# Kernel optimization log

Hardware: AMD Instinct MI355X
Metric: run time of the kernel (lower is better)

The kernel has to match this reference:

```python
import jax, jax.numpy as jnp
import numpy as np

N_NODES = 50000
N_EDGES = 800000
D = 64            # NODE_FEATURE_DIM == EDGE_FEATURE_DIM
H = 128           # EDGE_FEATURE_HIDDEN
EDGE_STEPS = 4
NODE_STEPS = 2


def _mlp2(h, W1, b1, W2, b2):
    # two-layer MLP with ReLU between (bn=False, end_with_relu=False)
    return jnp.maximum(h @ W1 + b1, 0.0) @ W2 + b2


def setup_inputs() -> dict:
    key = jax.random.key(0)
    ks = iter(jax.random.split(key, 40))

    def w(shape):
        fan_in = shape[0]
        return jax.random.normal(next(ks), shape, dtype=jnp.float32) / np.sqrt(fan_in)

    inp = {
        "x": jax.random.normal(next(ks), (N_NODES, 128), dtype=jnp.float32),
        "edge_attr": jax.random.normal(next(ks), (N_EDGES, 19), dtype=jnp.float32),
        "edge_index": jax.random.randint(next(ks), (2, N_EDGES), 0, N_NODES),
        "node_types": jax.random.randint(next(ks), (N_NODES,), 0, 17),
        # node embedding MLP: 128 -> 64 -> 64
        "ne_W1": w((128, D)), "ne_b1": jnp.zeros((D,)), "ne_W2": w((D, D)), "ne_b2": jnp.zeros((D,)),
        # edge embedding MLP: 19 -> 64 -> 64
        "ee_W1": w((19, D)), "ee_b1": jnp.zeros((D,)), "ee_W2": w((D, D)), "ee_b2": jnp.zeros((D,)),
        # MPN edge MLP: [x_src(2D), x_dst(2D), e(2D)] = 384 -> 128 -> 64
        "mp_eW1": w((6 * D, H)), "mp_eb1": jnp.zeros((H,)), "mp_eW2": w((H, D)), "mp_eb2": jnp.zeros((D,)),
        # MPN node-update MLP: 64 -> 64
        "mp_nW": w((D, D)), "mp_nb": jnp.zeros((D,)),
        # edge classification head: 64 -> 32 -> 1
        "ec_W1": w((D, 32)), "ec_b1": jnp.zeros((32,)), "ec_W2": w((32, 1)), "ec_b2": jnp.zeros((1,)),
        # node classification head: 64 -> 32 -> 1
        "nc_W1": w((D, 32)), "nc_b1": jnp.zeros((32,)), "nc_W2": w((32, 1)), "nc_b2": jnp.zeros((1,)),
        # type classification head: 64 -> 32 -> 17
        "cl_W1": w((D, 32)), "cl_b1": jnp.zeros((32,)), "cl_W2": w((32, 17)), "cl_b2": jnp.zeros((17,)),
    }
    return inp


def reference(x, edge_attr, edge_index, node_types,
              ne_W1, ne_b1, ne_W2, ne_b2,
              ee_W1, ee_b1, ee_W2, ee_b2,
              mp_eW1, mp_eb1, mp_eW2, mp_eb2,
              mp_nW, mp_nb,
              ec_W1, ec_b1, ec_W2, ec_b2,
              nc_W1, nc_b1, nc_W2, nc_b2,
              cl_W1, cl_b1, cl_W2, cl_b2):
    src, dst = edge_index[0], edge_index[1]

    nf0 = _mlp2(x, ne_W1, ne_b1, ne_W2, ne_b2)          # [N, D] initial node emb
    ef0 = _mlp2(edge_attr, ee_W1, ee_b1, ee_W2, ee_b2)  # [E, D] initial edge emb
    nf, ef = nf0, ef0

    def mpn_step(nf, ef):
        # skip connections: concat initial features each iteration
        nf_c = jnp.concatenate([nf0, nf], axis=1)   # [N, 2D]
        ef_c = jnp.concatenate([ef0, ef], axis=1)   # [E, 2D]
        msg_in = jnp.concatenate([nf_c[src], nf_c[dst], ef_c], axis=1)  # [E, 6D]
        e_new = _mlp2(msg_in, mp_eW1, mp_eb1, mp_eW2, mp_eb2)           # [E, D]
        agg = jax.ops.segment_sum(e_new, dst, num_segments=N_NODES)    # [N, D]
        n_new = jnp.maximum(agg @ mp_nW + mp_nb, 0.0)                   # [N, D]
        return n_new, e_new

    for _ in range(EDGE_STEPS):
        nf, ef = mpn_step(nf, ef)
    pred_edge = _mlp2(ef, ec_W1, ec_b1, ec_W2, ec_b2).squeeze(-1)  # [E]

    for _ in range(NODE_STEPS):
        nf, ef = mpn_step(nf, ef)
    pred_node = _mlp2(nf, nc_W1, nc_b1, nc_W2, nc_b2).squeeze(-1)  # [N]
    pred_class = _mlp2(nf, cl_W1, cl_b1, cl_W2, cl_b2)             # [N, 17]

    return (pred_edge, pred_node, pred_class)
```

## Files before the change

kernel.cpp:

```cpp
#include <hip/hip_runtime.h>

#define NN 50000
#define EE 800000

typedef unsigned short u16;
typedef __attribute__((ext_vector_type(8))) short bf16x8;
typedef __attribute__((ext_vector_type(4))) float f32x4;

#define MFMA16(a, b, c) __builtin_amdgcn_mfma_f32_16x16x32_bf16(a, b, c, 0, 0, 0)

__device__ __forceinline__ float bf2f(u16 v) {
    union { unsigned u; float f; } x; x.u = ((unsigned)v) << 16; return x.f;
}
__device__ __forceinline__ u16 f2bf(float f) {
    union { float f; unsigned u; } x; x.f = f;
    unsigned r = x.u + 0x7FFFu + ((x.u >> 16) & 1u);
    return (u16)(r >> 16);
}
__device__ __forceinline__ void gl_lds16(const u16* g, u16* l) {
    __builtin_amdgcn_global_load_lds((const __attribute__((address_space(1))) void*)g,
                                     (__attribute__((address_space(3))) void*)l, 16, 0, 0);
}

__global__ void pack_frag(const float* __restrict__ W, u16* __restrict__ dst, int K, int N) {
    int i = blockIdx.x * 256 + threadIdx.x;
    int nfc = N / 16, kkc = (K + 31) / 32;
    int total = kkc * nfc * 512;
    if (i >= total) return;
    int t = i & 7, lane = (i >> 3) & 63;
    int rest = i >> 9;
    int nf = rest % nfc, kk = rest / nfc;
    int k = kk * 32 + (lane >> 4) * 8 + t, n = nf * 16 + (lane & 15);
    dst[i] = (k < K) ? f2bf(W[k * N + n]) : (u16)0;
}

__global__ __launch_bounds__(256) void embed_mfma_node(
    const float* __restrict__ x, const u16* __restrict__ pW1, const float* __restrict__ b1,
    const u16* __restrict__ pW2, const float* __restrict__ b2, u16* __restrict__ out)
{
    __shared__ alignas(16) u16 A[64 * 136];
    __shared__ alignas(16) u16 Hs[64 * 72];
    int tid = threadIdx.x;
    size_t row0 = (size_t)blockIdx.x * 64;
    #pragma unroll
    for (int it = 0; it < 8; ++it) {
        int u = it * 256 + tid;
        int row = u >> 5, seg = u & 31;
        float4 v = (row0 + row < NN) ? *(const float4*)(x + (row0 + row) * 128 + seg * 4)
                                     : make_float4(0.f, 0.f, 0.f, 0.f);
        ushort4 o; o.x = f2bf(v.x); o.y = f2bf(v.y); o.z = f2bf(v.z); o.w = f2bf(v.w);
        *(ushort4*)(A + row * 136 + seg * 4) = o;
    }
    __syncthreads();
    int wave = tid >> 6, lane = tid & 63, l15 = lane & 15, l4 = lane >> 4;
    int col = wave * 16 + l15;
    f32x4 acc[4] = {};
    #pragma unroll
    for (int kk = 0; kk < 4; ++kk) {
        bf16x8 b = *(const bf16x8*)(pW1 + (size_t)((kk * 4 + wave) * 64 + lane) * 8);
        #pragma unroll
        for (int mi = 0; mi < 4; ++mi) {
            bf16x8 a = *(const bf16x8*)(A + (mi * 16 + l15) * 136 + kk * 32 + l4 * 8);
            acc[mi] = MFMA16(a, b, acc[mi]);
        }
    }
    float bias = b1[col];
    #pragma unroll
    for (int mi = 0; mi < 4; ++mi)
        #pragma unroll
        for (int r = 0; r < 4; ++r) {
            float v = acc[mi][r] + bias;
            Hs[(mi * 16 + l4 * 4 + r) * 72 + col] = f2bf(v > 0.f ? v : 0.f);
        }
    __syncthreads();
    f32x4 acc2[4] = {};
    #pragma unroll
    for (int kk = 0; kk < 2; ++kk) {
        bf16x8 b = *(const bf16x8*)(pW2 + (size_t)((kk * 4 + wave) * 64 + lane) * 8);
        #pragma unroll
        for (int mi = 0; mi < 4; ++mi) {
            bf16x8 a = *(const bf16x8*)(Hs + (mi * 16 + l15) * 72 + kk * 32 + l4 * 8);
            acc2[mi] = MFMA16(a, b, acc2[mi]);
        }
    }
    float bias2 = b2[col];
    __syncthreads();
    #pragma unroll
    for (int mi = 0; mi < 4; ++mi)
        #pragma unroll
        for (int r = 0; r < 4; ++r)
            Hs[(mi * 16 + l4 * 4 + r) * 72 + col] = f2bf(acc2[mi][r] + bias2);
    __syncthreads();
    #pragma unroll
    for (int it = 0; it < 4; ++it) {
        int u = it * 256 + tid;
        int row = u >> 4, c4 = (u & 15) * 4;
        if (row0 + row < NN) {
            ushort4 o = *(const ushort4*)(Hs + row * 72 + c4);
            *(ushort4*)(out + (row0 + row) * 64 + c4) = o;
        }
    }
}

__global__ __launch_bounds__(256) void embed_mfma_edge(
    const float* __restrict__ ea, const int* __restrict__ eids,
    const u16* __restrict__ pW1, const float* __restrict__ b1,
    const u16* __restrict__ pW2, const float* __restrict__ b2, u16* __restrict__ out)
{
    __shared__ alignas(16) u16 A[64 * 40];
    __shared__ alignas(16) u16 Hs[64 * 72];
    __shared__ int eid_s[64];
    int tid = threadIdx.x;
    size_t row0 = (size_t)blockIdx.x * 64;
    if (tid < 64) eid_s[tid] = eids[row0 + tid];
    __syncthreads();
    #pragma unroll
    for (int it = 0; it < 8; ++it) {
        int u = it * 256 + tid;
        int row = u >> 5, k = u & 31;
        float v = (k < 19) ? ea[(size_t)eid_s[row] * 19 + k] : 0.f;
        A[row * 40 + k] = f2bf(v);
    }
    __syncthreads();
    int wave = tid >> 6, lane = tid & 63, l15 = lane & 15, l4 = lane >> 4;
    int col = wave * 16 + l15;
    f32x4 acc[4] = {};
    {
        bf16x8 b = *(const bf16x8*)(pW1 + (size_t)(wave * 64 + lane) * 8);
        #pragma unroll
        for (int mi = 0; mi < 4; ++mi) {
            bf16x8 a = *(const bf16x8*)(A + (mi * 16 + l15) * 40 + l4 * 8);
            acc[mi] = MFMA16(a, b, acc[mi]);
        }
    }
    float bias = b1[col];
    #pragma unroll
    for (int mi = 0; mi < 4; ++mi)
        #pragma unroll
        for (int r = 0; r < 4; ++r) {
            float v = acc[mi][r] + bias;
            Hs[(mi * 16 + l4 * 4 + r) * 72 + col] = f2bf(v > 0.f ? v : 0.f);
        }
    __syncthreads();
    f32x4 acc2[4] = {};
    #pragma unroll
    for (int kk = 0; kk < 2; ++kk) {
        bf16x8 b = *(const bf16x8*)(pW2 + (size_t)((kk * 4 + wave) * 64 + lane) * 8);
        #pragma unroll
        for (int mi = 0; mi < 4; ++mi) {
            bf16x8 a = *(const bf16x8*)(Hs + (mi * 16 + l15) * 72 + kk * 32 + l4 * 8);
            acc2[mi] = MFMA16(a, b, acc2[mi]);
        }
    }
    float bias2 = b2[col];
    __syncthreads();
    #pragma unroll
    for (int mi = 0; mi < 4; ++mi)
        #pragma unroll
        for (int r = 0; r < 4; ++r)
            Hs[(mi * 16 + l4 * 4 + r) * 72 + col] = f2bf(acc2[mi][r] + bias2);
    __syncthreads();
    #pragma unroll
    for (int it = 0; it < 4; ++it) {
        int u = it * 256 + tid;
        int row = u >> 4, c4 = (u & 15) * 4;
        ushort4 o = *(const ushort4*)(Hs + row * 72 + c4);
        *(ushort4*)(out + (row0 + row) * 64 + c4) = o;
    }
}

__global__ void zero_cnt(int* __restrict__ cnt) {
    int i = blockIdx.x * 256 + threadIdx.x;
    if (i < NN) cnt[i] = 0;
}
__global__ void count_deg(const int* __restrict__ eidx, int* __restrict__ cnt) {
    int e = blockIdx.x * 256 + threadIdx.x;
    if (e < EE) atomicAdd(&cnt[eidx[EE + e]], 1);
}
__global__ void scan_k(const int* __restrict__ cnt, int* __restrict__ starts) {
    __shared__ int part[1024];
    int t = threadIdx.x;
    const int chunk = (NN + 1023) / 1024;
    int lo = t * chunk, hi = lo + chunk; if (hi > NN) hi = NN;
    if (lo > NN) lo = NN;
    int s = 0;
    for (int i = lo; i < hi; ++i) s += cnt[i];
    part[t] = s;
    __syncthreads();
    for (int off = 1; off < 1024; off <<= 1) {
        int v = part[t];
        int add = (t >= off) ? part[t - off] : 0;
        __syncthreads();
        part[t] = v + add;
        __syncthreads();
    }
    int run = (t == 0) ? 0 : part[t - 1];
    for (int i = lo; i < hi; ++i) { starts[i] = run; run += cnt[i]; }
    if (t == 1023) starts[NN] = EE;
}
__global__ void init_cur(const int* __restrict__ starts, int* __restrict__ cur) {
    int i = blockIdx.x * 256 + threadIdx.x;
    if (i < NN) cur[i] = starts[i];
}
__global__ void scatter_e(const int* __restrict__ eidx, int* __restrict__ cur,
                          int* __restrict__ eids) {
    int e = blockIdx.x * 256 + threadIdx.x;
    if (e < EE) {
        int pos = atomicAdd(&cur[eidx[EE + e]], 1);
        eids[pos] = e;
    }
}
__global__ void build_perm(const int* __restrict__ eidx, const int* __restrict__ eids,
                           int* __restrict__ psrc, int* __restrict__ pdst) {
    int j = blockIdx.x * 256 + threadIdx.x;
    if (j < EE) {
        int e = eids[j];
        psrc[j] = eidx[e];
        pdst[j] = eidx[EE + e];
    }
}

__global__ __launch_bounds__(256, 3) void edge_mlp(
    const int* __restrict__ psrc, const int* __restrict__ pdst,
    const u16* __restrict__ nf0, const u16* __restrict__ nfc,
    const u16* __restrict__ ef0, const u16* __restrict__ efc,
    const u16* __restrict__ pW1, const u16* __restrict__ pW2,
    const float* __restrict__ eb1, const float* __restrict__ eb2,
    u16* __restrict__ efn,
    const int* __restrict__ eids, const u16* __restrict__ pcW1,
    const float* __restrict__ hb1, const float* __restrict__ hW2,
    const float* __restrict__ hb2, float* __restrict__ outE, int doHead)
{
    __shared__ alignas(16) u16 Chunk[6][64 * 64];
    const int tid = threadIdx.x;
    const int tile0 = blockIdx.x * 64;
    const int wave = tid >> 6, lane = tid & 63;
    const int l15 = lane & 15, l4 = lane >> 4;

    const int r0 = wave * 16 + (lane >> 3);
    const int r1 = r0 + 8;
    const int u_ = lane & 7;
    const int su0 = u_ ^ (r0 & 7);
    const int su1 = u_ ^ (r1 & 7);
    const int is0 = psrc[tile0 + r0] * 64;
    const int is1 = psrc[tile0 + r1] * 64;
    const int id0 = pdst[tile0 + r0] * 64;
    const int id1 = pdst[tile0 + r1] * 64;

    bf16x8 bw[24];
    #pragma unroll
    for (int kk = 0; kk < 12; ++kk) {
        bw[kk * 2 + 0] = *(const bf16x8*)(pW1 + (size_t)((kk * 8 + wave * 2 + 0) * 64 + lane) * 8);
        bw[kk * 2 + 1] = *(const bf16x8*)(pW1 + (size_t)((kk * 8 + wave * 2 + 1) * 64 + lane) * 8);
    }
    #pragma unroll
    for (int i = 0; i < 24; ++i) asm volatile("" : "+v"(bw[i]));
    __builtin_amdgcn_sched_barrier(0);

    #pragma unroll
    for (int c = 0; c < 6; ++c) {
        const u16 *b0, *b1;
        if (c == 0)      { b0 = nf0 + is0; b1 = nf0 + is1; }
        else if (c == 1) { b0 = nfc + is0; b1 = nfc + is1; }
        else if (c == 2) { b0 = nf0 + id0; b1 = nf0 + id1; }
        else if (c == 3) { b0 = nfc + id0; b1 = nfc + id1; }
        else if (c == 4) { b0 = ef0 + (size_t)(tile0 + r0) * 64; b1 = ef0 + (size_t)(tile0 + r1) * 64; }
        else             { b0 = efc + (size_t)(tile0 + r0) * 64; b1 = efc + (size_t)(tile0 + r1) * 64; }
        u16* l0 = (u16*)Chunk + c * 4096 + wave * 1024;
        gl_lds16(b0 + su0 * 8, l0);
        gl_lds16(b1 + su1 * 8, l0 + 512);
    }
    __builtin_amdgcn_sched_barrier(0);

    f32x4 acc[4][2] = {};
    #pragma unroll
    for (int c = 0; c < 6; ++c) {
        if (c == 0)      asm volatile("s_waitcnt vmcnt(10)" ::: "memory");
        else if (c == 1) asm volatile("s_waitcnt vmcnt(8)" ::: "memory");
        else if (c == 2) asm volatile("s_waitcnt vmcnt(6)" ::: "memory");
        else if (c == 3) asm volatile("s_waitcnt vmcnt(4)" ::: "memory");
        else if (c == 4) asm volatile("s_waitcnt vmcnt(2)" ::: "memory");
        else             asm volatile("s_waitcnt vmcnt(0)" ::: "memory");
        __builtin_amdgcn_s_barrier();
        __builtin_amdgcn_sched_barrier(0);
        const char* Cb = (const char*)Chunk + c * 8192;
        #pragma unroll
        for (int kkl = 0; kkl < 2; ++kkl) {
            const int kk = c * 2 + kkl;
            #pragma unroll
            for (int mi = 0; mi < 4; ++mi) {
                int row = mi * 16 + l15;
                bf16x8 a = *(const bf16x8*)(Cb + row * 128 + ((kkl * 64 + l4 * 16) ^ ((row & 7) << 4)));
                acc[mi][0] = MFMA16(a, bw[kk * 2 + 0], acc[mi][0]);
                acc[mi][1] = MFMA16(a, bw[kk * 2 + 1], acc[mi][1]);
            }
        }
    }
    #pragma unroll
    for (int i = 0; i < 24; ++i) asm volatile("" : "+v"(bw[i]));

    char* HidB = (char*)Chunk;
    #pragma unroll
    for (int nj = 0; nj < 2; ++nj) {
        int col = wave * 32 + nj * 16 + l15;
        float bias = eb1[col];
        #pragma unroll
        for (int mi = 0; mi < 4; ++mi) {
            #pragma unroll
            for (int r = 0; r < 4; ++r) {
                int row = mi * 16 + l4 * 4 + r;
                float v = acc[mi][nj][r] + bias;
                v = v > 0.f ? v : 0.f;
                *(u16*)(HidB + row * 256 + ((col * 2) ^ ((row & 7) << 4))) = f2bf(v);
            }
        }
    }
    __syncthreads();

    f32x4 acc2[4] = {};
    const int m0 = wave * 16;
    #pragma unroll
    for (int kk = 0; kk < 4; ++kk) {
        int row = m0 + l15;
        bf16x8 a = *(const bf16x8*)(HidB + row * 256 + ((kk * 64 + l4 * 16) ^ ((row & 7) << 4)));
        #pragma unroll
        for (int nf = 0; nf < 4; ++nf) {
            bf16x8 b = *(const bf16x8*)(pW2 + (size_t)((kk * 4 + nf) * 64 + lane) * 8);
            acc2[nf] = MFMA16(a, b, acc2[nf]);
        }
    }

    float* EnF = (float*)((char*)Chunk + 16384);
    #pragma unroll
    for (int nf = 0; nf < 4; ++nf) {
        int col = nf * 16 + l15;
        float bias = eb2[col];
        #pragma unroll
        for (int r = 0; r < 4; ++r) {
            int row = m0 + l4 * 4 + r;
            EnF[row * 68 + col] = acc2[nf][r] + bias;
        }
    }
    __syncthreads();
    #pragma unroll
    for (int rep = 0; rep < 4; ++rep) {
        int u = rep * 256 + tid;
        int el = u >> 4, d0 = (u & 15) * 4;
        const float* s = EnF + el * 68 + d0;
        ushort4 o;
        o.x = f2bf(s[0]); o.y = f2bf(s[1]); o.z = f2bf(s[2]); o.w = f2bf(s[3]);
        *(ushort4*)(efn + (size_t)(tile0 + el) * 64 + d0) = o;
    }

    if (doHead) {
        f32x4 hacc[2] = {};
        #pragma unroll
        for (int kk = 0; kk < 2; ++kk) {
            const float* s = EnF + (m0 + l15) * 68 + kk * 32 + l4 * 8;
            bf16x8 a;
            #pragma unroll
            for (int j = 0; j < 8; ++j) a[j] = (short)f2bf(s[j]);
            #pragma unroll
            for (int nf = 0; nf < 2; ++nf) {
                bf16x8 b = *(const bf16x8*)(pcW1 + (size_t)((kk * 2 + nf) * 64 + lane) * 8);
                hacc[nf] = MFMA16(a, b, hacc[nf]);
            }
        }
        float bias2 = hb2[0];
        #pragma unroll
        for (int r = 0; r < 4; ++r) {
            float p = 0.f;
            #pragma unroll
            for (int nf = 0; nf < 2; ++nf) {
                int col = nf * 16 + l15;
                float h = hacc[nf][r] + hb1[col];
                p += (h > 0.f ? h : 0.f) * hW2[col];
            }
            p += __shfl_xor(p, 1); p += __shfl_xor(p, 2);
            p += __shfl_xor(p, 4); p += __shfl_xor(p, 8);
            if (l15 == 0) outE[eids[tile0 + m0 + l4 * 4 + r]] = p + bias2;
        }
    }
}

__global__ __launch_bounds__(256) void node_update(
    const u16* __restrict__ enewp,
    const int* __restrict__ starts,
    const float* __restrict__ Wn, const float* __restrict__ bn,
    u16* __restrict__ nfn)
{
    __shared__ float Wns[64 * 64];
    int tid = threadIdx.x;
    for (int i = tid; i < 4096; i += 256) Wns[i] = Wn[i];
    __syncthreads();
    const int l = tid & 63;
    const int q = l & 15;
    const int base = l & 48;
    const int n = blockIdx.x * 16 + (tid >> 4);
    if (n >= NN) return;
    const int s0 = starts[n], s1 = starts[n + 1];
    const int cnt = s1 - s0;
    const u16* p = enewp + (size_t)s0 * 64 + q * 4;
    float a0 = 0.f, a1 = 0.f, a2 = 0.f, a3 = 0.f;
    int i = 0;
    for (; i + 4 <= cnt; i += 4) {
        ushort4 v0 = *(const ushort4*)(p + (i + 0) * 64);
        ushort4 v1 = *(const ushort4*)(p + (i + 1) * 64);
        ushort4 v2 = *(const ushort4*)(p + (i + 2) * 64);
        ushort4 v3 = *(const ushort4*)(p + (i + 3) * 64);
        a0 += bf2f(v0.x) + bf2f(v1.x) + bf2f(v2.x) + bf2f(v3.x);
        a1 += bf2f(v0.y) + bf2f(v1.y) + bf2f(v2.y) + bf2f(v3.y);
        a2 += bf2f(v0.z) + bf2f(v1.z) + bf2f(v2.z) + bf2f(v3.z);
        a3 += bf2f(v0.w) + bf2f(v1.w) + bf2f(v2.w) + bf2f(v3.w);
    }
    for (; i < cnt; ++i) {
        ushort4 v0 = *(const ushort4*)(p + i * 64);
        a0 += bf2f(v0.x); a1 += bf2f(v0.y); a2 += bf2f(v0.z); a3 += bf2f(v0.w);
    }
    const float4 bb = *(const float4*)(bn + q * 4);
    float o0 = bb.x, o1 = bb.y, o2 = bb.z, o3 = bb.w;
    #pragma unroll
    for (int hq = 0; hq < 16; ++hq) {
        int src = base | hq;
        float b0 = __shfl(a0, src), b1 = __shfl(a1, src);
        float b2 = __shfl(a2, src), b3 = __shfl(a3, src);
        const float4 w0 = *(const float4*)(Wns + (hq * 4 + 0) * 64 + q * 4);
        const float4 w1 = *(const float4*)(Wns + (hq * 4 + 1) * 64 + q * 4);
        const float4 w2 = *(const float4*)(Wns + (hq * 4 + 2) * 64 + q * 4);
        const float4 w3 = *(const float4*)(Wns + (hq * 4 + 3) * 64 + q * 4);
        o0 += b0 * w0.x + b1 * w1.x + b2 * w2.x + b3 * w3.x;
        o1 += b0 * w0.y + b1 * w1.y + b2 * w2.y + b3 * w3.y;
        o2 += b0 * w0.z + b1 * w1.z + b2 * w2.z + b3 * w3.z;
        o3 += b0 * w0.w + b1 * w1.w + b2 * w2.w + b3 * w3.w;
    }
    ushort4 o;
    o.x = f2bf(o0 > 0.f ? o0 : 0.f);
    o.y = f2bf(o1 > 0.f ? o1 : 0.f);
    o.z = f2bf(o2 > 0.f ? o2 : 0.f);
    o.w = f2bf(o3 > 0.f ? o3 : 0.f);
    *(ushort4*)(nfn + (size_t)n * 64 + q * 4) = o;
}

__global__ void node_head(const u16* __restrict__ nf,
                          const float* __restrict__ ncW1, const float* __restrict__ ncb1,
                          const float* __restrict__ ncW2, const float* __restrict__ ncb2,
                          const float* __restrict__ clW1, const float* __restrict__ clb1,
                          const float* __restrict__ clW2, const float* __restrict__ clb2,
                          float* __restrict__ outN, float* __restrict__ outC) {
    __shared__ float sNW1[2048], sCW1[2048], sCW2[32 * 17];
    __shared__ float sNb1[32], sCb1[32], sNW2[32], sCb2[17];
    int tid = threadIdx.x;
    for (int i = tid; i < 2048; i += 256) { sNW1[i] = ncW1[i]; sCW1[i] = clW1[i]; }
    for (int i = tid; i < 544; i += 256) sCW2[i] = clW2[i];
    if (tid < 32) { sNb1[tid] = ncb1[tid]; sCb1[tid] = clb1[tid]; sNW2[tid] = ncW2[tid]; }
    if (tid < 17) sCb2[tid] = clb2[tid];
    __syncthreads();
    int n = blockIdx.x * 256 + tid;
    if (n >= NN) return;
    const u16* r = nf + (size_t)n * 64;
    float v[64];
    for (int k4 = 0; k4 < 16; ++k4) {
        ushort4 q = *(const ushort4*)(r + k4 * 4);
        v[k4 * 4 + 0] = bf2f(q.x); v[k4 * 4 + 1] = bf2f(q.y);
        v[k4 * 4 + 2] = bf2f(q.z); v[k4 * 4 + 3] = bf2f(q.w);
    }
    float h[32];
    #pragma unroll
    for (int j = 0; j < 32; ++j) h[j] = sNb1[j];
    for (int k = 0; k < 64; ++k) {
        float vk = v[k];
        #pragma unroll
        for (int j = 0; j < 32; ++j) h[j] += vk * sNW1[k * 32 + j];
    }
    float o = ncb2[0];
    #pragma unroll
    for (int j = 0; j < 32; ++j) o += (h[j] > 0.f ? h[j] : 0.f) * sNW2[j];
    outN[n] = o;
    #pragma unroll
    for (int j = 0; j < 32; ++j) h[j] = sCb1[j];
    for (int k = 0; k < 64; ++k) {
        float vk = v[k];
        #pragma unroll
        for (int j = 0; j < 32; ++j) h[j] += vk * sCW1[k * 32 + j];
    }
    float oc[17];
    #pragma unroll
    for (int c = 0; c < 17; ++c) oc[c] = sCb2[c];
    #pragma unroll
    for (int j = 0; j < 32; ++j) {
        float hr = h[j] > 0.f ? h[j] : 0.f;
        #pragma unroll
        for (int c = 0; c < 17; ++c) oc[c] += hr * sCW2[j * 17 + c];
    }
    #pragma unroll
    for (int c = 0; c < 17; ++c) outC[(size_t)n * 17 + c] = oc[c];
}

extern "C" void kernel_launch(void* const* d_in, const int* in_sizes, int n_in,
                              void* d_out, int out_size, void* d_ws, size_t ws_size,
                              hipStream_t stream) {
    const float* x     = (const float*)d_in[0];
    const float* ea    = (const float*)d_in[1];
    const int*   eidx  = (const int*)d_in[2];
    const float* neW1  = (const float*)d_in[4];
    const float* neb1  = (const float*)d_in[5];
    const float* neW2  = (const float*)d_in[6];
    const float* neb2  = (const float*)d_in[7];
    const float* eeW1  = (const float*)d_in[8];
    const float* eeb1  = (const float*)d_in[9];
    const float* eeW2  = (const float*)d_in[10];
    const float* eeb2  = (const float*)d_in[11];
    const float* mpW1  = (const float*)d_in[12];
    const float* mpb1  = (const float*)d_in[13];
    const float* mpW2  = (const float*)d_in[14];
    const float* mpb2  = (const float*)d_in[15];
    const float* mpnW  = (const float*)d_in[16];
    const float* mpnb  = (const float*)d_in[17];
    const float* ecW1  = (const float*)d_in[18];
    const float* ecb1  = (const float*)d_in[19];
    const float* ecW2  = (const float*)d_in[20];
    const float* ecb2  = (const float*)d_in[21];
    const float* ncW1  = (const float*)d_in[22];
    const float* ncb1  = (const float*)d_in[23];
    const float* ncW2  = (const float*)d_in[24];
    const float* ncb2  = (const float*)d_in[25];
    const float* clW1  = (const float*)d_in[26];
    const float* clb1  = (const float*)d_in[27];
    const float* clW2  = (const float*)d_in[28];
    const float* clb2  = (const float*)d_in[29];

    char* w = (char*)d_ws;
    size_t used = 0;
    auto alloc = [&](size_t b) {
        char* p = w + used; used += (b + 255) & ~(size_t)255; return p;
    };
    u16* nf0  = (u16*)alloc((size_t)NN * 64 * 2);
    u16* nfW  = (u16*)alloc((size_t)NN * 64 * 2);
    u16* ef0  = (u16*)alloc((size_t)EE * 64 * 2);
    u16* efW  = (u16*)alloc((size_t)EE * 64 * 2);
    u16* pmW1 = (u16*)alloc(49152 * 2);
    u16* pmW2 = (u16*)alloc(8192 * 2);
    u16* pnW1 = (u16*)alloc(8192 * 2);
    u16* pnW2 = (u16*)alloc(4096 * 2);
    u16* peW1 = (u16*)alloc(2048 * 2);
    u16* peW2 = (u16*)alloc(4096 * 2);
    u16* pcW1 = (u16*)alloc(2048 * 2);
    int* cnt    = (int*)alloc((size_t)NN * 4);
    int* starts = (int*)alloc((size_t)(NN + 1) * 4);
    int* eids   = (int*)alloc((size_t)EE * 4);
    int* psrc   = (int*)alloc((size_t)EE * 4);
    int* pdst   = (int*)alloc((size_t)EE * 4);
    if (used > ws_size) return;

    pack_frag<<<192, 256, 0, stream>>>(mpW1, pmW1, 384, 128);
    pack_frag<<<32, 256, 0, stream>>>(mpW2, pmW2, 128, 64);
    pack_frag<<<32, 256, 0, stream>>>(neW1, pnW1, 128, 64);
    pack_frag<<<16, 256, 0, stream>>>(neW2, pnW2, 64, 64);
    pack_frag<<<8, 256, 0, stream>>>(eeW1, peW1, 19, 64);
    pack_frag<<<16, 256, 0, stream>>>(eeW2, peW2, 64, 64);
    pack_frag<<<8, 256, 0, stream>>>(ecW1, pcW1, 64, 32);

    zero_cnt<<<(NN + 255) / 256, 256, 0, stream>>>(cnt);
    count_deg<<<EE / 256, 256, 0, stream>>>(eidx, cnt);
    scan_k<<<1, 1024, 0, stream>>>(cnt, starts);
    init_cur<<<(NN + 255) / 256, 256, 0, stream>>>(starts, cnt);
    scatter_e<<<EE / 256, 256, 0, stream>>>(eidx, cnt, eids);
    build_perm<<<EE / 256, 256, 0, stream>>>(eidx, eids, psrc, pdst);

    embed_mfma_node<<<(NN + 63) / 64, 256, 0, stream>>>(x, pnW1, neb1, pnW2, neb2, nf0);
    embed_mfma_edge<<<EE / 64, 256, 0, stream>>>(ea, eids, peW1, eeb1, peW2, eeb2, ef0);

    float* outE = (float*)d_out;
    float* outN = outE + EE;
    float* outC = outN + NN;

    const u16* nfc = nf0;
    const u16* efc = ef0;
    for (int s = 0; s < 6; ++s) {
        edge_mlp<<<EE / 64, 256, 0, stream>>>(psrc, pdst, nf0, nfc, ef0, efc,
                                              pmW1, pmW2, mpb1, mpb2, efW,
                                              eids, pcW1, ecb1, ecW2, ecb2, outE,
                                              (s == 3) ? 1 : 0);
        node_update<<<(NN + 15) / 16, 256, 0, stream>>>(efW, starts, mpnW, mpnb, nfW);
        efc = efW;
        nfc = nfW;
    }
    node_head<<<(NN + 255) / 256, 256, 0, stream>>>(nfc, ncW1, ncb1, ncW2, ncb2,
                                                    clW1, clb1, clW2, clb2, outN, outC);
    (void)in_sizes; (void)n_in; (void)out_size;
}
```

Baseline: 1.235 ms.

## Interleave initial and current features into single 128-wide node and edge buffers

Node and edge features are stored as one 128-column row per node or edge: the initial embedding in the first half and the current step's features in the second half. The edge MLP now gathers both halves of each source and destination row from adjacent memory. Each step writes the new halves in place, so the per-step pointer swapping and the separate work buffers go away. It also drops an asm register pin on the weight fragments after the first GEMM. In exchange, node_update reads edge rows at a 256-byte stride instead of densely, and the embed kernels write each value twice.

Result: no change. 1.253 ms (+1.5%).

```diff
diff --git a/kernel.cpp b/kernel.cpp
--- a/kernel.cpp
+++ b/kernel.cpp
@@ -97,7 +97,8 @@
         int row = u >> 4, c4 = (u & 15) * 4;
         if (row0 + row < NN) {
             ushort4 o = *(const ushort4*)(Hs + row * 72 + c4);
-            *(ushort4*)(out + (row0 + row) * 64 + c4) = o;
+            *(ushort4*)(out + (row0 + row) * 128 + c4) = o;
+            *(ushort4*)(out + (row0 + row) * 128 + 64 + c4) = o;
         }
     }
 }
@@ -165,7 +166,8 @@
         int u = it * 256 + tid;
         int row = u >> 4, c4 = (u & 15) * 4;
         ushort4 o = *(const ushort4*)(Hs + row * 72 + c4);
-        *(ushort4*)(out + (row0 + row) * 64 + c4) = o;
+        *(ushort4*)(out + (row0 + row) * 128 + c4) = o;
+        *(ushort4*)(out + (row0 + row) * 128 + 64 + c4) = o;
     }
 }
 
@@ -222,11 +224,9 @@
 
 __global__ __launch_bounds__(256, 3) void edge_mlp(
     const int* __restrict__ psrc, const int* __restrict__ pdst,
-    const u16* __restrict__ nf0, const u16* __restrict__ nfc,
-    const u16* __restrict__ ef0, const u16* __restrict__ efc,
+    const u16* __restrict__ nfI, u16* __restrict__ eF,
     const u16* __restrict__ pW1, const u16* __restrict__ pW2,
     const float* __restrict__ eb1, const float* __restrict__ eb2,
-    u16* __restrict__ efn,
     const int* __restrict__ eids, const u16* __restrict__ pcW1,
     const float* __restrict__ hb1, const float* __restrict__ hW2,
     const float* __restrict__ hb2, float* __restrict__ outE, int doHead)
@@ -242,10 +242,12 @@
     const int u_ = lane & 7;
     const int su0 = u_ ^ (r0 & 7);
     const int su1 = u_ ^ (r1 & 7);
-    const int is0 = psrc[tile0 + r0] * 64;
-    const int is1 = psrc[tile0 + r1] * 64;
-    const int id0 = pdst[tile0 + r0] * 64;
-    const int id1 = pdst[tile0 + r1] * 64;
+    const size_t is0 = (size_t)psrc[tile0 + r0] * 128;
+    const size_t is1 = (size_t)psrc[tile0 + r1] * 128;
+    const size_t id0 = (size_t)pdst[tile0 + r0] * 128;
+    const size_t id1 = (size_t)pdst[tile0 + r1] * 128;
+    const size_t ie0 = (size_t)(tile0 + r0) * 128;
+    const size_t ie1 = (size_t)(tile0 + r1) * 128;
 
     bf16x8 bw[24];
     #pragma unroll
@@ -260,12 +262,12 @@
     #pragma unroll
     for (int c = 0; c < 6; ++c) {
         const u16 *b0, *b1;
-        if (c == 0)      { b0 = nf0 + is0; b1 = nf0 + is1; }
-        else if (c == 1) { b0 = nfc + is0; b1 = nfc + is1; }
-        else if (c == 2) { b0 = nf0 + id0; b1 = nf0 + id1; }
-        else if (c == 3) { b0 = nfc + id0; b1 = nfc + id1; }
-        else if (c == 4) { b0 = ef0 + (size_t)(tile0 + r0) * 64; b1 = ef0 + (size_t)(tile0 + r1) * 64; }
-        else             { b0 = efc + (size_t)(tile0 + r0) * 64; b1 = efc + (size_t)(tile0 + r1) * 64; }
+        if (c == 0)      { b0 = nfI + is0;      b1 = nfI + is1; }
+        else if (c == 1) { b0 = nfI + is0 + 64; b1 = nfI + is1 + 64; }
+        else if (c == 2) { b0 = nfI + id0;      b1 = nfI + id1; }
+        else if (c == 3) { b0 = nfI + id0 + 64; b1 = nfI + id1 + 64; }
+        else if (c == 4) { b0 = eF + ie0;       b1 = eF + ie1; }
+        else             { b0 = eF + ie0 + 64;  b1 = eF + ie1 + 64; }
         u16* l0 = (u16*)Chunk + c * 4096 + wave * 1024;
         gl_lds16(b0 + su0 * 8, l0);
         gl_lds16(b1 + su1 * 8, l0 + 512);
@@ -296,8 +298,6 @@
             }
         }
     }
-    #pragma unroll
-    for (int i = 0; i < 24; ++i) asm volatile("" : "+v"(bw[i]));
 
     char* HidB = (char*)Chunk;
     #pragma unroll
@@ -349,7 +349,7 @@
         const float* s = EnF + el * 68 + d0;
         ushort4 o;
         o.x = f2bf(s[0]); o.y = f2bf(s[1]); o.z = f2bf(s[2]); o.w = f2bf(s[3]);
-        *(ushort4*)(efn + (size_t)(tile0 + el) * 64 + d0) = o;
+        *(ushort4*)(eF + (size_t)(tile0 + el) * 128 + 64 + d0) = o;
     }
 
     if (doHead) {
@@ -384,10 +384,10 @@
 }
 
 __global__ __launch_bounds__(256) void node_update(
-    const u16* __restrict__ enewp,
+    const u16* __restrict__ eF,
     const int* __restrict__ starts,
     const float* __restrict__ Wn, const float* __restrict__ bn,
-    u16* __restrict__ nfn)
+    u16* __restrict__ nfI)
 {
     __shared__ float Wns[64 * 64];
     int tid = threadIdx.x;
@@ -400,21 +400,21 @@
     if (n >= NN) return;
     const int s0 = starts[n], s1 = starts[n + 1];
     const int cnt = s1 - s0;
-    const u16* p = enewp + (size_t)s0 * 64 + q * 4;
+    const u16* p = eF + (size_t)s0 * 128 + 64 + q * 4;
     float a0 = 0.f, a1 = 0.f, a2 = 0.f, a3 = 0.f;
     int i = 0;
     for (; i + 4 <= cnt; i += 4) {
-        ushort4 v0 = *(const ushort4*)(p + (i + 0) * 64);
-        ushort4 v1 = *(const ushort4*)(p + (i + 1) * 64);
-        ushort4 v2 = *(const ushort4*)(p + (i + 2) * 64);
-        ushort4 v3 = *(const ushort4*)(p + (i + 3) * 64);
+        ushort4 v0 = *(const ushort4*)(p + (i + 0) * 128);
+        ushort4 v1 = *(const ushort4*)(p + (i + 1) * 128);
+        ushort4 v2 = *(const ushort4*)(p + (i + 2) * 128);
+        ushort4 v3 = *(const ushort4*)(p + (i + 3) * 128);
         a0 += bf2f(v0.x) + bf2f(v1.x) + bf2f(v2.x) + bf2f(v3.x);
         a1 += bf2f(v0.y) + bf2f(v1.y) + bf2f(v2.y) + bf2f(v3.y);
         a2 += bf2f(v0.z) + bf2f(v1.z) + bf2f(v2.z) + bf2f(v3.z);
         a3 += bf2f(v0.w) + bf2f(v1.w) + bf2f(v2.w) + bf2f(v3.w);
     }
     for (; i < cnt; ++i) {
-        ushort4 v0 = *(const ushort4*)(p + i * 64);
+        ushort4 v0 = *(const ushort4*)(p + i * 128);
         a0 += bf2f(v0.x); a1 += bf2f(v0.y); a2 += bf2f(v0.z); a3 += bf2f(v0.w);
     }
     const float4 bb = *(const float4*)(bn + q * 4);
@@ -438,10 +438,10 @@
     o.y = f2bf(o1 > 0.f ? o1 : 0.f);
     o.z = f2bf(o2 > 0.f ? o2 : 0.f);
     o.w = f2bf(o3 > 0.f ? o3 : 0.f);
-    *(ushort4*)(nfn + (size_t)n * 64 + q * 4) = o;
-}
-
-__global__ void node_head(const u16* __restrict__ nf,
+    *(ushort4*)(nfI + (size_t)n * 128 + 64 + q * 4) = o;
+}
+
+__global__ void node_head(const u16* __restrict__ nfI,
                           const float* __restrict__ ncW1, const float* __restrict__ ncb1,
                           const float* __restrict__ ncW2, const float* __restrict__ ncb2,
                           const float* __restrict__ clW1, const float* __restrict__ clb1,
@@ -457,7 +457,7 @@
     __syncthreads();
     int n = blockIdx.x * 256 + tid;
     if (n >= NN) return;
-    const u16* r = nf + (size_t)n * 64;
+    const u16* r = nfI + (size_t)n * 128 + 64;
     float v[64];
     for (int k4 = 0; k4 < 16; ++k4) {
         ushort4 q = *(const ushort4*)(r + k4 * 4);
@@ -534,10 +534,8 @@
     auto alloc = [&](size_t b) {
         char* p = w + used; used += (b + 255) & ~(size_t)255; return p;
     };
-    u16* nf0  = (u16*)alloc((size_t)NN * 64 * 2);
-    u16* nfW  = (u16*)alloc((size_t)NN * 64 * 2);
-    u16* ef0  = (u16*)alloc((size_t)EE * 64 * 2);
-    u16* efW  = (u16*)alloc((size_t)EE * 64 * 2);
+    u16* nfI  = (u16*)alloc((size_t)NN * 128 * 2);
+    u16* eF   = (u16*)alloc((size_t)EE * 128 * 2);
     u16* pmW1 = (u16*)alloc(49152 * 2);
     u16* pmW2 = (u16*)alloc(8192 * 2);
     u16* pnW1 = (u16*)alloc(8192 * 2);
@@ -567,25 +565,21 @@
     scatter_e<<<EE / 256, 256, 0, stream>>>(eidx, cnt, eids);
     build_perm<<<EE / 256, 256, 0, stream>>>(eidx, eids, psrc, pdst);
 
-    embed_mfma_node<<<(NN + 63) / 64, 256, 0, stream>>>(x, pnW1, neb1, pnW2, neb2, nf0);
-    embed_mfma_edge<<<EE / 64, 256, 0, stream>>>(ea, eids, peW1, eeb1, peW2, eeb2, ef0);
+    embed_mfma_node<<<(NN + 63) / 64, 256, 0, stream>>>(x, pnW1, neb1, pnW2, neb2, nfI);
+    embed_mfma_edge<<<EE / 64, 256, 0, stream>>>(ea, eids, peW1, eeb1, peW2, eeb2, eF);
 
     float* outE = (float*)d_out;
     float* outN = outE + EE;
     float* outC = outN + NN;
 
-    const u16* nfc = nf0;
-    const u16* efc = ef0;
     for (int s = 0; s < 6; ++s) {
-        edge_mlp<<<EE / 64, 256, 0, stream>>>(psrc, pdst, nf0, nfc, ef0, efc,
-                                              pmW1, pmW2, mpb1, mpb2, efW,
+        edge_mlp<<<EE / 64, 256, 0, stream>>>(psrc, pdst, nfI, eF,
+                                              pmW1, pmW2, mpb1, mpb2,
                                               eids, pcW1, ecb1, ecW2, ecb2, outE,
                                               (s == 3) ? 1 : 0);
-        node_update<<<(NN + 15) / 16, 256, 0, stream>>>(efW, starts, mpnW, mpnb, nfW);
-        efc = efW;
-        nfc = nfW;
-    }
-    node_head<<<(NN + 255) / 256, 256, 0, stream>>>(nfc, ncW1, ncb1, ncW2, ncb2,
+        node_update<<<(NN + 15) / 16, 256, 0, stream>>>(eF, starts, mpnW, mpnb, nfI);
+    }
+    node_head<<<(NN + 255) / 256, 256, 0, stream>>>(nfI, ncW1, ncb1, ncW2, ncb2,
                                                     clW1, clb1, clW2, clb2, outN, outC);
     (void)in_sizes; (void)n_in; (void)out_size;
 }
```
